# Performance work log

Measured on AMD Instinct MI355X. Metric: run time of the kernel, lower is better.

## Reference

```python
import jax, jax.numpy as jnp
import numpy as np

N_NODES = 50000
N_EDGES = 1600000
IN_FEATS = 128
HIDDEN = 128
N_CLASSES = 16
N_GRAPHS = 512


def setup_inputs() -> dict:
    key = jax.random.key(0)
    ks = jax.random.split(key, 10)
    features = jax.random.normal(ks[0], (N_NODES, IN_FEATS), dtype=jnp.float32)
    src = jax.random.randint(ks[1], (N_EDGES,), 0, N_NODES, dtype=jnp.int32)
    dst = jax.random.randint(ks[2], (N_EDGES,), 0, N_NODES, dtype=jnp.int32)
    graph_ids = jnp.sort(jax.random.randint(ks[3], (N_NODES,), 0, N_GRAPHS, dtype=jnp.int32))
    # GraphConv weights (glorot-ish scaling) and biases
    W1 = jax.random.normal(ks[4], (IN_FEATS, HIDDEN), dtype=jnp.float32) / np.sqrt(IN_FEATS)
    b1 = jnp.zeros((HIDDEN,), dtype=jnp.float32)
    W2 = jax.random.normal(ks[5], (HIDDEN, HIDDEN), dtype=jnp.float32) / np.sqrt(HIDDEN)
    b2 = jnp.zeros((HIDDEN,), dtype=jnp.float32)
    Wf = jax.random.normal(ks[6], (HIDDEN, N_CLASSES), dtype=jnp.float32) / np.sqrt(HIDDEN)
    bf = jnp.zeros((N_CLASSES,), dtype=jnp.float32)
    return {"features": features, "W1": W1, "b1": b1, "W2": W2, "b2": b2,
            "Wf": Wf, "bf": bf, "src": src, "dst": dst, "graph_ids": graph_ids}


def _graph_conv(h, W, b, src, dst, norm_out, norm_in):
    # DGL GraphConv, norm='both': h' = D_in^{-1/2} * A^T * (D_out^{-1/2} * h) @ W + b
    h = h * norm_out[:, None]              # [N, d] scale by src out-degree
    agg = jax.ops.segment_sum(h[src], dst, num_segments=N_NODES)  # gather-scatter SpMM
    agg = agg * norm_in[:, None]
    return agg @ W + b


def reference(features, W1, b1, W2, b2, Wf, bf, src, dst, graph_ids):
    ones_e = jnp.ones((N_EDGES,), dtype=features.dtype)
    deg_out = jax.ops.segment_sum(ones_e, src, num_segments=N_NODES)
    deg_in = jax.ops.segment_sum(ones_e, dst, num_segments=N_NODES)
    norm_out = jnp.where(deg_out > 0, jax.lax.rsqrt(jnp.maximum(deg_out, 1.0)), 0.0)
    norm_in = jnp.where(deg_in > 0, jax.lax.rsqrt(jnp.maximum(deg_in, 1.0)), 0.0)

    x = jax.nn.relu(_graph_conv(features, W1, b1, src, dst, norm_out, norm_in))
    x = jax.nn.relu(_graph_conv(x, W2, b2, src, dst, norm_out, norm_in))

    # mean_nodes: per-graph mean pooling over batched graph
    sums = jax.ops.segment_sum(x, graph_ids, num_segments=N_GRAPHS)   # [G, d]
    counts = jax.ops.segment_sum(jnp.ones((N_NODES,), dtype=x.dtype), graph_ids,
                                 num_segments=N_GRAPHS)
    pooled = sums / jnp.maximum(counts, 1.0)[:, None]
    return pooled @ Wf + bf
```

## Files before the change

### kernel.cpp

```cpp
#include <hip/hip_runtime.h>

#define N_NODES 50000
#define N_EDGES 1600000
#define FEATS 128
#define N_GRAPHS 512
#define N_CLASSES 16

#define NC 400
#define CE 4000
#define NB 391
#define SLAB 4608
#define CSLAB 5632
#define ZROW 50000

typedef __attribute__((ext_vector_type(8))) short bf16x8;
typedef __attribute__((ext_vector_type(4))) float f32x4;

__device__ inline unsigned bf16_rne_bits(float x) {
    unsigned u = __float_as_uint(x);
    return (u + 0x7FFFu + ((u >> 16) & 1u)) >> 16;
}
__device__ inline unsigned pack_bf16(float a, float b) {
    return (bf16_rne_bits(b) << 16) | bf16_rne_bits(a);
}
__device__ inline float bf16lo(unsigned u) { return __uint_as_float(u << 16); }
__device__ inline float bf16hi(unsigned u) { return __uint_as_float(u & 0xFFFF0000u); }

__global__ __launch_bounds__(256) void countrank_kernel(
        const int* __restrict__ src, const int* __restrict__ dst,
        unsigned* __restrict__ ranks, unsigned* __restrict__ cntD, unsigned* __restrict__ cntS,
        const float* __restrict__ W1, const float* __restrict__ W2,
        unsigned short* __restrict__ t1h, unsigned short* __restrict__ t1l,
        unsigned short* __restrict__ t2h, unsigned short* __restrict__ t2l) {
    __shared__ unsigned hD[NB], hS[NB];
    if (blockIdx.x >= NC) {
        int b = blockIdx.x - NC;
        const float* W = (b < 64) ? W1 : W2;
        unsigned short* th = (b < 64) ? t1h : t2h;
        unsigned short* tl = (b < 64) ? t1l : t2l;
        int idx = (b & 63) * 256 + threadIdx.x;
        int k = idx >> 7;
        int col = idx & 127;
        float w = W[idx];
        unsigned hb = bf16_rne_bits(w);
        float hf = __uint_as_float(hb << 16);
        unsigned lb = bf16_rne_bits(w - hf);
        th[col * 128 + k] = (unsigned short)hb;
        tl[col * 128 + k] = (unsigned short)lb;
        return;
    }
    for (int i = threadIdx.x; i < NB; i += 256) { hD[i] = 0; hS[i] = 0; }
    __syncthreads();
    int c = blockIdx.x;
    int lo = c * CE;
    for (int i = lo + threadIdx.x; i < lo + CE; i += 256) {
        int d = dst[i];
        int s = src[i];
        unsigned rD = atomicAdd(&hD[d >> 7], 1u);
        unsigned rS = atomicAdd(&hS[s >> 7], 1u);
        ranks[i] = rD | (rS << 16);
    }
    __syncthreads();
    for (int i = threadIdx.x; i < NB; i += 256) {
        cntD[c * NB + i] = hD[i];
        cntS[c * NB + i] = hS[i];
    }
}

__global__ __launch_bounds__(512) void colscan_kernel(
        unsigned* __restrict__ cntD, unsigned* __restrict__ cntS,
        unsigned* __restrict__ totD, unsigned* __restrict__ totS) {
    int bb = blockIdx.x;
    unsigned* cnt = (bb < NB) ? cntD : cntS;
    unsigned* tot = (bb < NB) ? totD : totS;
    int col = (bb < NB) ? bb : bb - NB;
    __shared__ unsigned buf[512];
    int t = threadIdx.x;
    unsigned v = (t < NC) ? cnt[t * NB + col] : 0;
    buf[t] = v;
    __syncthreads();
    for (int off = 1; off < 512; off <<= 1) {
        unsigned add = (t >= off) ? buf[t - off] : 0;
        __syncthreads();
        buf[t] += add;
        __syncthreads();
    }
    if (t < NC) cnt[t * NB + col] = buf[t] - v;
    if (t == NC - 1) tot[col] = buf[t];
}

__global__ __launch_bounds__(256) void scatter_kernel(
        const int* __restrict__ src, const int* __restrict__ dst,
        const unsigned* __restrict__ ranks,
        const unsigned* __restrict__ colbaseD, const unsigned* __restrict__ colbaseS,
        unsigned* __restrict__ arenaD, unsigned char* __restrict__ arenaS) {
    __shared__ unsigned cbD[NB], cbS[NB];
    int c = blockIdx.x;
    for (int i = threadIdx.x; i < NB; i += 256) {
        cbD[i] = colbaseD[c * NB + i];
        cbS[i] = colbaseS[c * NB + i];
    }
    __syncthreads();
    int lo = c * CE;
    for (int i = lo + threadIdx.x; i < lo + CE; i += 256) {
        int d = dst[i];
        int s = src[i];
        unsigned rr = ranks[i];
        unsigned posD = (unsigned)(d >> 7) * SLAB + cbD[d >> 7] + (rr & 0xFFFFu);
        arenaD[posD] = (unsigned)s | ((unsigned)(d & 127) << 16);
        unsigned posS = (unsigned)(s >> 7) * SLAB + cbS[s >> 7] + (rr >> 16);
        arenaS[posS] = (unsigned char)(s & 127);
    }
}

__global__ __launch_bounds__(256) void finalize_kernel(
        const unsigned* __restrict__ arenaD, const unsigned* __restrict__ totD,
        const unsigned char* __restrict__ arenaS, const unsigned* __restrict__ totS,
        unsigned short* __restrict__ csr, unsigned* __restrict__ row_start,
        unsigned* __restrict__ cnt_in, unsigned* __restrict__ deg_out) {
    int b = blockIdx.x;
    __shared__ unsigned h[128], h2[128], loc[128], sbuf[128];
    __shared__ unsigned short stag[CSLAB];
    int t = threadIdx.x;
    if (t < 128) { h[t] = 0; h2[t] = 0; }
    for (int i = t; i < CSLAB; i += 256) stag[i] = (unsigned short)ZROW;
    __syncthreads();
    unsigned nbS = totS[b];
    const unsigned char* slabS = arenaS + (size_t)b * SLAB;
    for (unsigned i = t; i < nbS; i += 256) atomicAdd(&h2[slabS[i]], 1u);
    __syncthreads();
    if (t < 128) {
        int ss = b * 128 + t;
        if (ss < N_NODES) deg_out[ss] = h2[t];
        h2[t] = 0;
    }
    __syncthreads();
    unsigned nb = totD[b];
    const unsigned* slab = arenaD + (size_t)b * SLAB;
    for (unsigned i = t; i < nb; i += 256) atomicAdd(&h[slab[i] >> 16], 1u);
    __syncthreads();
    unsigned myv = 0;
    if (t < 128) { myv = (h[t] + 7u) & ~7u; sbuf[t] = myv; }
    __syncthreads();
    for (int off = 1; off < 128; off <<= 1) {
        unsigned add = 0;
        if (t < 128 && t >= off) add = sbuf[t - off];
        __syncthreads();
        if (t < 128) sbuf[t] += add;
        __syncthreads();
    }
    if (t < 128) {
        loc[t] = sbuf[t] - myv;
        int dd = b * 128 + t;
        if (dd < N_NODES) {
            cnt_in[dd] = h[t];
            row_start[dd] = (unsigned)b * CSLAB + loc[t];
        }
    }
    __syncthreads();
    for (unsigned i = t; i < nb; i += 256) {
        unsigned e = slab[i];
        unsigned dl = e >> 16;
        unsigned r = atomicAdd(&h2[dl], 1u);
        stag[loc[dl] + r] = (unsigned short)(e & 0xFFFFu);
    }
    __syncthreads();
    unsigned tot_aligned = sbuf[127];
    unsigned short* g = csr + (size_t)b * CSLAB;
    for (unsigned i = t; i < tot_aligned; i += 256) g[i] = stag[i];
}

__global__ void norm_prescale_kernel(const unsigned* __restrict__ deg_out,
                                     const unsigned* __restrict__ cnt_in,
                                     const float* __restrict__ X, unsigned* __restrict__ Xs,
                                     float* __restrict__ norm_in_a, float* __restrict__ norm_out_a,
                                     const int* __restrict__ gids,
                                     int* __restrict__ gstart, int* __restrict__ gend) {
    int gid = blockIdx.x * blockDim.x + threadIdx.x;
    if (gid >= (N_NODES + 1) * 16) return;
    int node = gid >> 4;
    int c = gid & 15;
    if (node >= N_NODES) {
        uint4 z = {0u, 0u, 0u, 0u};
        *reinterpret_cast<uint4*>(Xs + (size_t)node * (FEATS / 2) + c * 4) = z;
        return;
    }
    unsigned d0 = deg_out[node];
    float no = d0 > 0 ? rsqrtf((float)d0) : 0.f;
    float4 a0 = *reinterpret_cast<const float4*>(X + (size_t)node * FEATS + c * 8);
    float4 a1 = *reinterpret_cast<const float4*>(X + (size_t)node * FEATS + c * 8 + 4);
    uint4 p;
    p.x = pack_bf16(a0.x * no, a0.y * no);
    p.y = pack_bf16(a0.z * no, a0.w * no);
    p.z = pack_bf16(a1.x * no, a1.y * no);
    p.w = pack_bf16(a1.z * no, a1.w * no);
    *reinterpret_cast<uint4*>(Xs + (size_t)node * (FEATS / 2) + c * 4) = p;
    if (c == 0) {
        norm_out_a[node] = no;
        unsigned d1 = cnt_in[node];
        norm_in_a[node] = d1 > 0 ? rsqrtf((float)d1) : 0.f;
        int g = gids[node];
        if (node == 0 || gids[node - 1] != g) gstart[g] = node;
        if (node == N_NODES - 1 || gids[node + 1] != g) gend[g] = node + 1;
    }
}

__global__ __launch_bounds__(256) void agg_kernel(const unsigned* __restrict__ Xs,
        const unsigned short* __restrict__ csr, const unsigned* __restrict__ row_start,
        const unsigned* __restrict__ cnt_in, unsigned* __restrict__ out) {
    int b = blockIdx.x;
    int h = b & 1;
    int node = (b >> 1) * 8 + (threadIdx.x >> 5);
    if (node >= N_NODES) return;
    int lane = threadIdx.x & 31;
    unsigned n = cnt_in[node];
    const unsigned short* row = csr + row_start[node];
    const unsigned base = h * 32 + lane;
    float alo = 0.f, ahi = 0.f;
    unsigned n8 = (n + 7u) & ~7u;
    for (unsigned j = 0; j < n8; j += 8) {
        uint4 iv = *reinterpret_cast<const uint4*>(row + j);
        unsigned s0 = iv.x & 0xFFFFu, s1 = iv.x >> 16;
        unsigned s2 = iv.y & 0xFFFFu, s3 = iv.y >> 16;
        unsigned s4 = iv.z & 0xFFFFu, s5 = iv.z >> 16;
        unsigned s6 = iv.w & 0xFFFFu, s7 = iv.w >> 16;
        unsigned g0 = Xs[(size_t)s0 * 64 + base];
        unsigned g1 = Xs[(size_t)s1 * 64 + base];
        unsigned g2 = Xs[(size_t)s2 * 64 + base];
        unsigned g3 = Xs[(size_t)s3 * 64 + base];
        unsigned g4 = Xs[(size_t)s4 * 64 + base];
        unsigned g5 = Xs[(size_t)s5 * 64 + base];
        unsigned g6 = Xs[(size_t)s6 * 64 + base];
        unsigned g7 = Xs[(size_t)s7 * 64 + base];
        alo += ((bf16lo(g0) + bf16lo(g1)) + (bf16lo(g2) + bf16lo(g3)))
             + ((bf16lo(g4) + bf16lo(g5)) + (bf16lo(g6) + bf16lo(g7)));
        ahi += ((bf16hi(g0) + bf16hi(g1)) + (bf16hi(g2) + bf16hi(g3)))
             + ((bf16hi(g4) + bf16hi(g5)) + (bf16hi(g6) + bf16hi(g7)));
    }
    out[(size_t)node * 64 + base] = pack_bf16(alo, ahi);
}

template <bool BF16_OUT>
__global__ __launch_bounds__(256) void gemm_kernel(
        const unsigned* __restrict__ A,
        const unsigned short* __restrict__ Wth, const unsigned short* __restrict__ Wtl,
        const float* __restrict__ bias, const float* __restrict__ norm_in,
        const float* __restrict__ post, float* __restrict__ out_f32,
        unsigned short* __restrict__ out_b16, int n_rows) {
    __shared__ unsigned sWh[128 * 68];
    __shared__ unsigned sWl[128 * 68];
    {
        const uint4* gh = reinterpret_cast<const uint4*>(Wth);
        const uint4* gl = reinterpret_cast<const uint4*>(Wtl);
        for (int i = threadIdx.x; i < 2048; i += 256) {
            int col = i >> 4, q = i & 15;
            *reinterpret_cast<uint4*>(sWh + col * 68 + q * 4) = gh[i];
            *reinterpret_cast<uint4*>(sWl + col * 68 + q * 4) = gl[i];
        }
    }
    __syncthreads();

    const int l = threadIdx.x & 63;
    const int w = threadIdx.x >> 6;
    const int rl = l & 15;
    const int kg = l >> 4;
    const int row0 = blockIdx.x * 64 + w * 16;

    int row_a = row0 + rl;
    if (row_a >= n_rows) row_a = n_rows - 1;
    const uint4* Arow = reinterpret_cast<const uint4*>(A + (size_t)row_a * 64);

    f32x4 acc[8];
#pragma unroll
    for (int ct = 0; ct < 8; ++ct) acc[ct] = (f32x4){0.f, 0.f, 0.f, 0.f};

#pragma unroll
    for (int s = 0; s < 4; ++s) {
        bf16x8 af = __builtin_bit_cast(bf16x8, Arow[4 * s + kg]);
#pragma unroll
        for (int ct = 0; ct < 8; ++ct) {
            int colb = ct * 16 + rl;
            bf16x8 bh = __builtin_bit_cast(bf16x8,
                *reinterpret_cast<const uint4*>(sWh + colb * 68 + 16 * s + 4 * kg));
            bf16x8 bl = __builtin_bit_cast(bf16x8,
                *reinterpret_cast<const uint4*>(sWl + colb * 68 + 16 * s + 4 * kg));
            acc[ct] = __builtin_amdgcn_mfma_f32_16x16x32_bf16(af, bl, acc[ct], 0, 0, 0);
            acc[ct] = __builtin_amdgcn_mfma_f32_16x16x32_bf16(af, bh, acc[ct], 0, 0, 0);
        }
    }

    const int rb = row0 + kg * 4;
    float ni[4], po[4];
#pragma unroll
    for (int j = 0; j < 4; ++j) {
        int r = rb + j;
        bool v = r < n_rows;
        ni[j] = v ? norm_in[r] : 0.f;
        po[j] = (BF16_OUT && v) ? post[r] : 1.f;
    }
#pragma unroll
    for (int ct = 0; ct < 8; ++ct) {
        int col = ct * 16 + rl;
        float bc = bias[col];
#pragma unroll
        for (int j = 0; j < 4; ++j) {
            int r = rb + j;
            if (r < n_rows) {
                float o = fmaxf(fmaf(acc[ct][j], ni[j], bc), 0.f);
                if (BF16_OUT)
                    out_b16[(size_t)r * 128 + col] = (unsigned short)bf16_rne_bits(o * po[j]);
                else
                    out_f32[(size_t)r * 128 + col] = o;
            }
        }
    }
}

__global__ __launch_bounds__(256) void pool_final_kernel(
        const float* __restrict__ H, const int* __restrict__ gstart,
        const int* __restrict__ gend, const float* __restrict__ Wf,
        const float* __restrict__ bf, float* __restrict__ out) {
    int g = blockIdx.x;
    int s = gstart[g];
    int e = gend[g];
    int f = threadIdx.x & 127;
    int h = threadIdx.x >> 7;
    float acc = 0.f;
    for (int r = s + h; r < e; r += 2) acc += H[(size_t)r * FEATS + f];
    __shared__ float tmp[256];
    __shared__ float pooled[FEATS];
    tmp[threadIdx.x] = acc;
    __syncthreads();
    if (threadIdx.x < FEATS) {
        float inv = 1.0f / fmaxf((float)(e - s), 1.0f);
        pooled[threadIdx.x] = (tmp[threadIdx.x] + tmp[threadIdx.x + 128]) * inv;
    }
    __syncthreads();
    if (threadIdx.x < N_CLASSES) {
        int c = threadIdx.x;
        float d = bf[c];
        for (int k = 0; k < FEATS; ++k) d = fmaf(pooled[k], Wf[k * N_CLASSES + c], d);
        out[g * N_CLASSES + c] = d;
    }
}

extern "C" void kernel_launch(void* const* d_in, const int* in_sizes, int n_in,
                              void* d_out, int out_size, void* d_ws, size_t ws_size,
                              hipStream_t stream) {
    const float* features = (const float*)d_in[0];
    const float* W1 = (const float*)d_in[1];
    const float* b1 = (const float*)d_in[2];
    const float* W2 = (const float*)d_in[3];
    const float* b2 = (const float*)d_in[4];
    const float* Wf = (const float*)d_in[5];
    const float* bf = (const float*)d_in[6];
    const int* src = (const int*)d_in[7];
    const int* dst = (const int*)d_in[8];
    const int* gids = (const int*)d_in[9];
    float* out = (float*)d_out;

    char* wp = (char*)d_ws;
    auto alloc = [&wp](size_t bytes) {
        char* p = wp;
        wp += (bytes + 255) & ~(size_t)255;
        return p;
    };
    unsigned* buf0u = (unsigned*)alloc(((size_t)N_NODES + 1) * 64 * 4);
    float* buf1 = (float*)alloc((size_t)N_NODES * FEATS * 4 + 256);
    unsigned* B16 = (unsigned*)buf1;
    unsigned short* B16s = (unsigned short*)buf1;
    float* norm_in_a = (float*)alloc(N_NODES * 4);
    float* norm_out_a = (float*)alloc(N_NODES * 4);
    unsigned* deg_out = (unsigned*)alloc(N_NODES * 4);
    unsigned* cnt_in = (unsigned*)alloc(N_NODES * 4);
    unsigned* row_start = (unsigned*)alloc(N_NODES * 4);
    int* gboth = (int*)alloc(2 * N_GRAPHS * 4);
    int* gstart = gboth;
    int* gend = gboth + N_GRAPHS;
    unsigned short* t1h = (unsigned short*)alloc(4 * 16384 * 2);
    unsigned short* t1l = t1h + 16384;
    unsigned short* t2h = t1l + 16384;
    unsigned short* t2l = t2h + 16384;
    unsigned* cntD = (unsigned*)alloc((size_t)NC * NB * 4);
    unsigned* cntS = (unsigned*)alloc((size_t)NC * NB * 4);
    unsigned* totD = (unsigned*)alloc(NB * 4);
    unsigned* totS = (unsigned*)alloc(NB * 4);
    unsigned* arenaD = (unsigned*)alloc((size_t)NB * SLAB * 4);
    unsigned* ranks = (unsigned*)alloc((size_t)N_EDGES * 4);
    unsigned short* csr = (unsigned short*)ranks;
    unsigned char* arenaS = (unsigned char*)alloc((size_t)NB * SLAB);

    (void)hipMemsetAsync(gboth, 0, 2 * N_GRAPHS * sizeof(int), stream);

    countrank_kernel<<<NC + 128, 256, 0, stream>>>(src, dst, ranks, cntD, cntS,
                                                   W1, W2, t1h, t1l, t2h, t2l);
    colscan_kernel<<<2 * NB, 512, 0, stream>>>(cntD, cntS, totD, totS);
    scatter_kernel<<<NC, 256, 0, stream>>>(src, dst, ranks, cntD, cntS, arenaD, arenaS);
    finalize_kernel<<<NB, 256, 0, stream>>>(arenaD, totD, arenaS, totS,
                                            csr, row_start, cnt_in, deg_out);

    norm_prescale_kernel<<<((N_NODES + 1) * 16 + 255) / 256, 256, 0, stream>>>(
        deg_out, cnt_in, features, B16, norm_in_a, norm_out_a, gids, gstart, gend);

    const int agg_blocks = 2 * ((N_NODES + 7) / 8);
    const int gemm_blocks = (N_NODES + 63) / 64;

    agg_kernel<<<agg_blocks, 256, 0, stream>>>(B16, csr, row_start, cnt_in, buf0u);
    gemm_kernel<true><<<gemm_blocks, 256, 0, stream>>>(
        buf0u, t1h, t1l, b1, norm_in_a, norm_out_a, nullptr, B16s, N_NODES);

    agg_kernel<<<agg_blocks, 256, 0, stream>>>(B16, csr, row_start, cnt_in, buf0u);
    gemm_kernel<false><<<gemm_blocks, 256, 0, stream>>>(
        buf0u, t2h, t2l, b2, norm_in_a, nullptr, buf1, nullptr, N_NODES);

    pool_final_kernel<<<N_GRAPHS, 256, 0, stream>>>(buf1, gstart, gend, Wf, bf, out);
}
```

Measured before the change: 219.5 us.

## Split CSR rows by source half and widen aggregation gathers to uint2

The CSR build now partitions each destination row into two padded segments, one for sources below a midpoint and one for sources above. Both in-degree counts are packed into a single word. The aggregation kernel now gives each node 16 lanes, and each lane loads two packed words (four bf16 values) per neighbour. This halves gather instruction count and may improve cache locality by grouping source ranges. The cost is extra padding entries, which means more zero-row gathers and a tighter fit in the fixed CSLAB staging area.

Result: slower. 226.0 us (+2.9%).

```diff
diff --git a/kernel.cpp b/kernel.cpp
--- a/kernel.cpp
+++ b/kernel.cpp
@@ -12,6 +12,7 @@
 #define SLAB 4608
 #define CSLAB 5632
 #define ZROW 50000
+#define SRC_MID 25000
 
 typedef __attribute__((ext_vector_type(8))) short bf16x8;
 typedef __attribute__((ext_vector_type(4))) float f32x4;
@@ -117,30 +118,37 @@
         const unsigned* __restrict__ arenaD, const unsigned* __restrict__ totD,
         const unsigned char* __restrict__ arenaS, const unsigned* __restrict__ totS,
         unsigned short* __restrict__ csr, unsigned* __restrict__ row_start,
-        unsigned* __restrict__ cnt_in, unsigned* __restrict__ deg_out) {
+        unsigned* __restrict__ cnt2, unsigned* __restrict__ deg_out) {
     int b = blockIdx.x;
-    __shared__ unsigned h[128], h2[128], loc[128], sbuf[128];
+    __shared__ unsigned hlo[128], hhi[128], clo[128], chi[128], loc[128], sbuf[128];
     __shared__ unsigned short stag[CSLAB];
     int t = threadIdx.x;
-    if (t < 128) { h[t] = 0; h2[t] = 0; }
+    if (t < 128) { hlo[t] = 0; hhi[t] = 0; clo[t] = 0; chi[t] = 0; }
     for (int i = t; i < CSLAB; i += 256) stag[i] = (unsigned short)ZROW;
     __syncthreads();
     unsigned nbS = totS[b];
     const unsigned char* slabS = arenaS + (size_t)b * SLAB;
-    for (unsigned i = t; i < nbS; i += 256) atomicAdd(&h2[slabS[i]], 1u);
+    for (unsigned i = t; i < nbS; i += 256) atomicAdd(&clo[slabS[i]], 1u);
     __syncthreads();
     if (t < 128) {
         int ss = b * 128 + t;
-        if (ss < N_NODES) deg_out[ss] = h2[t];
-        h2[t] = 0;
+        if (ss < N_NODES) deg_out[ss] = clo[t];
+        clo[t] = 0;
     }
     __syncthreads();
     unsigned nb = totD[b];
     const unsigned* slab = arenaD + (size_t)b * SLAB;
-    for (unsigned i = t; i < nb; i += 256) atomicAdd(&h[slab[i] >> 16], 1u);
+    for (unsigned i = t; i < nb; i += 256) {
+        unsigned e = slab[i];
+        if ((e & 0xFFFFu) < SRC_MID) atomicAdd(&hlo[e >> 16], 1u);
+        else atomicAdd(&hhi[e >> 16], 1u);
+    }
     __syncthreads();
     unsigned myv = 0;
-    if (t < 128) { myv = (h[t] + 7u) & ~7u; sbuf[t] = myv; }
+    if (t < 128) {
+        myv = ((hlo[t] + 7u) & ~7u) + ((hhi[t] + 7u) & ~7u);
+        sbuf[t] = myv;
+    }
     __syncthreads();
     for (int off = 1; off < 128; off <<= 1) {
         unsigned add = 0;
@@ -153,7 +161,7 @@
         loc[t] = sbuf[t] - myv;
         int dd = b * 128 + t;
         if (dd < N_NODES) {
-            cnt_in[dd] = h[t];
+            cnt2[dd] = hlo[t] | (hhi[t] << 16);
             row_start[dd] = (unsigned)b * CSLAB + loc[t];
         }
     }
@@ -161,8 +169,11 @@
     for (unsigned i = t; i < nb; i += 256) {
         unsigned e = slab[i];
         unsigned dl = e >> 16;
-        unsigned r = atomicAdd(&h2[dl], 1u);
-        stag[loc[dl] + r] = (unsigned short)(e & 0xFFFFu);
+        unsigned s = e & 0xFFFFu;
+        unsigned pos;
+        if (s < SRC_MID) pos = loc[dl] + atomicAdd(&clo[dl], 1u);
+        else pos = loc[dl] + ((hlo[dl] + 7u) & ~7u) + atomicAdd(&chi[dl], 1u);
+        stag[pos] = (unsigned short)s;
     }
     __syncthreads();
     unsigned tot_aligned = sbuf[127];
@@ -171,7 +182,7 @@
 }
 
 __global__ void norm_prescale_kernel(const unsigned* __restrict__ deg_out,
-                                     const unsigned* __restrict__ cnt_in,
+                                     const unsigned* __restrict__ cnt2,
                                      const float* __restrict__ X, unsigned* __restrict__ Xs,
                                      float* __restrict__ norm_in_a, float* __restrict__ norm_out_a,
                                      const int* __restrict__ gids,
@@ -197,7 +208,8 @@
     *reinterpret_cast<uint4*>(Xs + (size_t)node * (FEATS / 2) + c * 4) = p;
     if (c == 0) {
         norm_out_a[node] = no;
-        unsigned d1 = cnt_in[node];
+        unsigned c2 = cnt2[node];
+        unsigned d1 = (c2 & 0xFFFFu) + (c2 >> 16);
         norm_in_a[node] = d1 > 0 ? rsqrtf((float)d1) : 0.f;
         int g = gids[node];
         if (node == 0 || gids[node - 1] != g) gstart[g] = node;
@@ -207,37 +219,44 @@
 
 __global__ __launch_bounds__(256) void agg_kernel(const unsigned* __restrict__ Xs,
         const unsigned short* __restrict__ csr, const unsigned* __restrict__ row_start,
-        const unsigned* __restrict__ cnt_in, unsigned* __restrict__ out) {
+        const unsigned* __restrict__ cnt2, unsigned* __restrict__ out) {
     int b = blockIdx.x;
     int h = b & 1;
-    int node = (b >> 1) * 8 + (threadIdx.x >> 5);
+    int node = (b >> 1) * 16 + (threadIdx.x >> 4);
     if (node >= N_NODES) return;
-    int lane = threadIdx.x & 31;
-    unsigned n = cnt_in[node];
+    int lane = threadIdx.x & 15;
+    unsigned c2 = cnt2[node];
+    unsigned ntot = (((c2 & 0xFFFFu) + 7u) & ~7u) + (((c2 >> 16) + 7u) & ~7u);
     const unsigned short* row = csr + row_start[node];
-    const unsigned base = h * 32 + lane;
-    float alo = 0.f, ahi = 0.f;
-    unsigned n8 = (n + 7u) & ~7u;
-    for (unsigned j = 0; j < n8; j += 8) {
+    const unsigned base = h * 32 + lane * 2;
+    float a0 = 0.f, a1 = 0.f, a2 = 0.f, a3 = 0.f;
+    for (unsigned j = 0; j < ntot; j += 8) {
         uint4 iv = *reinterpret_cast<const uint4*>(row + j);
         unsigned s0 = iv.x & 0xFFFFu, s1 = iv.x >> 16;
         unsigned s2 = iv.y & 0xFFFFu, s3 = iv.y >> 16;
         unsigned s4 = iv.z & 0xFFFFu, s5 = iv.z >> 16;
         unsigned s6 = iv.w & 0xFFFFu, s7 = iv.w >> 16;
-        unsigned g0 = Xs[(size_t)s0 * 64 + base];
-        unsigned g1 = Xs[(size_t)s1 * 64 + base];
-        unsigned g2 = Xs[(size_t)s2 * 64 + base];
-        unsigned g3 = Xs[(size_t)s3 * 64 + base];
-        unsigned g4 = Xs[(size_t)s4 * 64 + base];
-        unsigned g5 = Xs[(size_t)s5 * 64 + base];
-        unsigned g6 = Xs[(size_t)s6 * 64 + base];
-        unsigned g7 = Xs[(size_t)s7 * 64 + base];
-        alo += ((bf16lo(g0) + bf16lo(g1)) + (bf16lo(g2) + bf16lo(g3)))
-             + ((bf16lo(g4) + bf16lo(g5)) + (bf16lo(g6) + bf16lo(g7)));
-        ahi += ((bf16hi(g0) + bf16hi(g1)) + (bf16hi(g2) + bf16hi(g3)))
-             + ((bf16hi(g4) + bf16hi(g5)) + (bf16hi(g6) + bf16hi(g7)));
-    }
-    out[(size_t)node * 64 + base] = pack_bf16(alo, ahi);
+        uint2 g0 = *reinterpret_cast<const uint2*>(Xs + (size_t)s0 * 64 + base);
+        uint2 g1 = *reinterpret_cast<const uint2*>(Xs + (size_t)s1 * 64 + base);
+        uint2 g2 = *reinterpret_cast<const uint2*>(Xs + (size_t)s2 * 64 + base);
+        uint2 g3 = *reinterpret_cast<const uint2*>(Xs + (size_t)s3 * 64 + base);
+        uint2 g4 = *reinterpret_cast<const uint2*>(Xs + (size_t)s4 * 64 + base);
+        uint2 g5 = *reinterpret_cast<const uint2*>(Xs + (size_t)s5 * 64 + base);
+        uint2 g6 = *reinterpret_cast<const uint2*>(Xs + (size_t)s6 * 64 + base);
+        uint2 g7 = *reinterpret_cast<const uint2*>(Xs + (size_t)s7 * 64 + base);
+        a0 += ((bf16lo(g0.x) + bf16lo(g1.x)) + (bf16lo(g2.x) + bf16lo(g3.x)))
+            + ((bf16lo(g4.x) + bf16lo(g5.x)) + (bf16lo(g6.x) + bf16lo(g7.x)));
+        a1 += ((bf16hi(g0.x) + bf16hi(g1.x)) + (bf16hi(g2.x) + bf16hi(g3.x)))
+            + ((bf16hi(g4.x) + bf16hi(g5.x)) + (bf16hi(g6.x) + bf16hi(g7.x)));
+        a2 += ((bf16lo(g0.y) + bf16lo(g1.y)) + (bf16lo(g2.y) + bf16lo(g3.y)))
+            + ((bf16lo(g4.y) + bf16lo(g5.y)) + (bf16lo(g6.y) + bf16lo(g7.y)));
+        a3 += ((bf16hi(g0.y) + bf16hi(g1.y)) + (bf16hi(g2.y) + bf16hi(g3.y)))
+            + ((bf16hi(g4.y) + bf16hi(g5.y)) + (bf16hi(g6.y) + bf16hi(g7.y)));
+    }
+    uint2 o;
+    o.x = pack_bf16(a0, a1);
+    o.y = pack_bf16(a2, a3);
+    *reinterpret_cast<uint2*>(out + (size_t)node * 64 + base) = o;
 }
 
 template <bool BF16_OUT>
@@ -372,7 +391,7 @@
     float* norm_in_a = (float*)alloc(N_NODES * 4);
     float* norm_out_a = (float*)alloc(N_NODES * 4);
     unsigned* deg_out = (unsigned*)alloc(N_NODES * 4);
-    unsigned* cnt_in = (unsigned*)alloc(N_NODES * 4);
+    unsigned* cnt2 = (unsigned*)alloc(N_NODES * 4);
     unsigned* row_start = (unsigned*)alloc(N_NODES * 4);
     int* gboth = (int*)alloc(2 * N_GRAPHS * 4);
     int* gstart = gboth;
@@ -397,19 +416,19 @@
     colscan_kernel<<<2 * NB, 512, 0, stream>>>(cntD, cntS, totD, totS);
     scatter_kernel<<<NC, 256, 0, stream>>>(src, dst, ranks, cntD, cntS, arenaD, arenaS);
     finalize_kernel<<<NB, 256, 0, stream>>>(arenaD, totD, arenaS, totS,
-                                            csr, row_start, cnt_in, deg_out);
+                                            csr, row_start, cnt2, deg_out);
 
     norm_prescale_kernel<<<((N_NODES + 1) * 16 + 255) / 256, 256, 0, stream>>>(
-        deg_out, cnt_in, features, B16, norm_in_a, norm_out_a, gids, gstart, gend);
-
-    const int agg_blocks = 2 * ((N_NODES + 7) / 8);
+        deg_out, cnt2, features, B16, norm_in_a, norm_out_a, gids, gstart, gend);
+
+    const int agg_blocks = 2 * ((N_NODES + 15) / 16);
     const int gemm_blocks = (N_NODES + 63) / 64;
 
-    agg_kernel<<<agg_blocks, 256, 0, stream>>>(B16, csr, row_start, cnt_in, buf0u);
+    agg_kernel<<<agg_blocks, 256, 0, stream>>>(B16, csr, row_start, cnt2, buf0u);
     gemm_kernel<true><<<gemm_blocks, 256, 0, stream>>>(
         buf0u, t1h, t1l, b1, norm_in_a, norm_out_a, nullptr, B16s, N_NODES);
 
-    agg_kernel<<<agg_blocks, 256, 0, stream>>>(B16, csr, row_start, cnt_in, buf0u);
+    agg_kernel<<<agg_blocks, 256, 0, stream>>>(B16, csr, row_start, cnt2, buf0u);
     gemm_kernel<false><<<gemm_blocks, 256, 0, stream>>>(
         buf0u, t2h, t2l, b2, norm_in_a, nullptr, buf1, nullptr, N_NODES);
 
```

## Fuse norm/prescale into finalize and split CSR rows by source half

Applied to the files above, without the earlier changes.

The norm_prescale kernel is merged into finalize_kernel, which now computes degrees, norms, graph bounds and the bf16 prescaled features per 128-node slab, removing one launch and the degree round trip through global memory. Each destination row's neighbor list is also split into two padded segments, sources below 25000 and sources at or above it, with both counts packed into one word. This groups gathers by source range to improve cache locality, at the cost of extra padding per row. The aggregation loop is unrolled by two.

Result: faster. 212.4 us (-3.2%).

```diff
diff --git a/kernel.cpp b/kernel.cpp
--- a/kernel.cpp
+++ b/kernel.cpp
@@ -12,6 +12,7 @@
 #define SLAB 4608
 #define CSLAB 5632
 #define ZROW 50000
+#define SRC_MID 25000
 
 typedef __attribute__((ext_vector_type(8))) short bf16x8;
 typedef __attribute__((ext_vector_type(4))) float f32x4;
@@ -117,30 +118,36 @@
         const unsigned* __restrict__ arenaD, const unsigned* __restrict__ totD,
         const unsigned char* __restrict__ arenaS, const unsigned* __restrict__ totS,
         unsigned short* __restrict__ csr, unsigned* __restrict__ row_start,
-        unsigned* __restrict__ cnt_in, unsigned* __restrict__ deg_out) {
+        unsigned* __restrict__ cnt2,
+        const float* __restrict__ X, unsigned* __restrict__ Xs,
+        float* __restrict__ norm_in_a, float* __restrict__ norm_out_a,
+        const int* __restrict__ gids, int* __restrict__ gstart, int* __restrict__ gend) {
     int b = blockIdx.x;
-    __shared__ unsigned h[128], h2[128], loc[128], sbuf[128];
+    __shared__ unsigned hlo[128], hhi[128], clo[128], chi[128], loc[128], sbuf[128], degs[128];
     __shared__ unsigned short stag[CSLAB];
     int t = threadIdx.x;
-    if (t < 128) { h[t] = 0; h2[t] = 0; }
+    if (t < 128) { hlo[t] = 0; hhi[t] = 0; clo[t] = 0; chi[t] = 0; }
     for (int i = t; i < CSLAB; i += 256) stag[i] = (unsigned short)ZROW;
     __syncthreads();
     unsigned nbS = totS[b];
     const unsigned char* slabS = arenaS + (size_t)b * SLAB;
-    for (unsigned i = t; i < nbS; i += 256) atomicAdd(&h2[slabS[i]], 1u);
-    __syncthreads();
-    if (t < 128) {
-        int ss = b * 128 + t;
-        if (ss < N_NODES) deg_out[ss] = h2[t];
-        h2[t] = 0;
-    }
+    for (unsigned i = t; i < nbS; i += 256) atomicAdd(&clo[slabS[i]], 1u);
+    __syncthreads();
+    if (t < 128) { degs[t] = clo[t]; clo[t] = 0; }
     __syncthreads();
     unsigned nb = totD[b];
     const unsigned* slab = arenaD + (size_t)b * SLAB;
-    for (unsigned i = t; i < nb; i += 256) atomicAdd(&h[slab[i] >> 16], 1u);
+    for (unsigned i = t; i < nb; i += 256) {
+        unsigned e = slab[i];
+        if ((e & 0xFFFFu) < SRC_MID) atomicAdd(&hlo[e >> 16], 1u);
+        else atomicAdd(&hhi[e >> 16], 1u);
+    }
     __syncthreads();
     unsigned myv = 0;
-    if (t < 128) { myv = (h[t] + 7u) & ~7u; sbuf[t] = myv; }
+    if (t < 128) {
+        myv = ((hlo[t] + 7u) & ~7u) + ((hhi[t] + 7u) & ~7u);
+        sbuf[t] = myv;
+    }
     __syncthreads();
     for (int off = 1; off < 128; off <<= 1) {
         unsigned add = 0;
@@ -153,7 +160,7 @@
         loc[t] = sbuf[t] - myv;
         int dd = b * 128 + t;
         if (dd < N_NODES) {
-            cnt_in[dd] = h[t];
+            cnt2[dd] = hlo[t] | (hhi[t] << 16);
             row_start[dd] = (unsigned)b * CSLAB + loc[t];
         }
     }
@@ -161,64 +168,65 @@
     for (unsigned i = t; i < nb; i += 256) {
         unsigned e = slab[i];
         unsigned dl = e >> 16;
-        unsigned r = atomicAdd(&h2[dl], 1u);
-        stag[loc[dl] + r] = (unsigned short)(e & 0xFFFFu);
+        unsigned s = e & 0xFFFFu;
+        unsigned pos;
+        if (s < SRC_MID) pos = loc[dl] + atomicAdd(&clo[dl], 1u);
+        else pos = loc[dl] + ((hlo[dl] + 7u) & ~7u) + atomicAdd(&chi[dl], 1u);
+        stag[pos] = (unsigned short)s;
     }
     __syncthreads();
     unsigned tot_aligned = sbuf[127];
     unsigned short* g = csr + (size_t)b * CSLAB;
     for (unsigned i = t; i < tot_aligned; i += 256) g[i] = stag[i];
-}
-
-__global__ void norm_prescale_kernel(const unsigned* __restrict__ deg_out,
-                                     const unsigned* __restrict__ cnt_in,
-                                     const float* __restrict__ X, unsigned* __restrict__ Xs,
-                                     float* __restrict__ norm_in_a, float* __restrict__ norm_out_a,
-                                     const int* __restrict__ gids,
-                                     int* __restrict__ gstart, int* __restrict__ gend) {
-    int gid = blockIdx.x * blockDim.x + threadIdx.x;
-    if (gid >= (N_NODES + 1) * 16) return;
-    int node = gid >> 4;
-    int c = gid & 15;
-    if (node >= N_NODES) {
-        uint4 z = {0u, 0u, 0u, 0u};
-        *reinterpret_cast<uint4*>(Xs + (size_t)node * (FEATS / 2) + c * 4) = z;
-        return;
-    }
-    unsigned d0 = deg_out[node];
-    float no = d0 > 0 ? rsqrtf((float)d0) : 0.f;
-    float4 a0 = *reinterpret_cast<const float4*>(X + (size_t)node * FEATS + c * 8);
-    float4 a1 = *reinterpret_cast<const float4*>(X + (size_t)node * FEATS + c * 8 + 4);
-    uint4 p;
-    p.x = pack_bf16(a0.x * no, a0.y * no);
-    p.y = pack_bf16(a0.z * no, a0.w * no);
-    p.z = pack_bf16(a1.x * no, a1.y * no);
-    p.w = pack_bf16(a1.z * no, a1.w * no);
-    *reinterpret_cast<uint4*>(Xs + (size_t)node * (FEATS / 2) + c * 4) = p;
-    if (c == 0) {
-        norm_out_a[node] = no;
-        unsigned d1 = cnt_in[node];
-        norm_in_a[node] = d1 > 0 ? rsqrtf((float)d1) : 0.f;
-        int g = gids[node];
-        if (node == 0 || gids[node - 1] != g) gstart[g] = node;
-        if (node == N_NODES - 1 || gids[node + 1] != g) gend[g] = node + 1;
+    for (int task = t; task < 128 * 16; task += 256) {
+        int nl = task >> 4;
+        int c = task & 15;
+        int node = b * 128 + nl;
+        if (node < N_NODES) {
+            unsigned d0 = degs[nl];
+            float no = d0 > 0 ? rsqrtf((float)d0) : 0.f;
+            float4 a0 = *reinterpret_cast<const float4*>(X + (size_t)node * FEATS + c * 8);
+            float4 a1 = *reinterpret_cast<const float4*>(X + (size_t)node * FEATS + c * 8 + 4);
+            uint4 p;
+            p.x = pack_bf16(a0.x * no, a0.y * no);
+            p.y = pack_bf16(a0.z * no, a0.w * no);
+            p.z = pack_bf16(a1.x * no, a1.y * no);
+            p.w = pack_bf16(a1.z * no, a1.w * no);
+            *reinterpret_cast<uint4*>(Xs + (size_t)node * (FEATS / 2) + c * 4) = p;
+        } else if (node == ZROW) {
+            uint4 z = {0u, 0u, 0u, 0u};
+            *reinterpret_cast<uint4*>(Xs + (size_t)node * (FEATS / 2) + c * 4) = z;
+        }
+    }
+    if (t < 128) {
+        int node = b * 128 + t;
+        if (node < N_NODES) {
+            unsigned d0 = degs[t];
+            norm_out_a[node] = d0 > 0 ? rsqrtf((float)d0) : 0.f;
+            unsigned d1 = hlo[t] + hhi[t];
+            norm_in_a[node] = d1 > 0 ? rsqrtf((float)d1) : 0.f;
+            int g2 = gids[node];
+            if (node == 0 || gids[node - 1] != g2) gstart[g2] = node;
+            if (node == N_NODES - 1 || gids[node + 1] != g2) gend[g2] = node + 1;
+        }
     }
 }
 
 __global__ __launch_bounds__(256) void agg_kernel(const unsigned* __restrict__ Xs,
         const unsigned short* __restrict__ csr, const unsigned* __restrict__ row_start,
-        const unsigned* __restrict__ cnt_in, unsigned* __restrict__ out) {
+        const unsigned* __restrict__ cnt2, unsigned* __restrict__ out) {
     int b = blockIdx.x;
     int h = b & 1;
     int node = (b >> 1) * 8 + (threadIdx.x >> 5);
     if (node >= N_NODES) return;
     int lane = threadIdx.x & 31;
-    unsigned n = cnt_in[node];
+    unsigned c2 = cnt2[node];
+    unsigned ntot = (((c2 & 0xFFFFu) + 7u) & ~7u) + (((c2 >> 16) + 7u) & ~7u);
     const unsigned short* row = csr + row_start[node];
     const unsigned base = h * 32 + lane;
     float alo = 0.f, ahi = 0.f;
-    unsigned n8 = (n + 7u) & ~7u;
-    for (unsigned j = 0; j < n8; j += 8) {
+#pragma unroll 2
+    for (unsigned j = 0; j < ntot; j += 8) {
         uint4 iv = *reinterpret_cast<const uint4*>(row + j);
         unsigned s0 = iv.x & 0xFFFFu, s1 = iv.x >> 16;
         unsigned s2 = iv.y & 0xFFFFu, s3 = iv.y >> 16;
@@ -371,8 +379,7 @@
     unsigned short* B16s = (unsigned short*)buf1;
     float* norm_in_a = (float*)alloc(N_NODES * 4);
     float* norm_out_a = (float*)alloc(N_NODES * 4);
-    unsigned* deg_out = (unsigned*)alloc(N_NODES * 4);
-    unsigned* cnt_in = (unsigned*)alloc(N_NODES * 4);
+    unsigned* cnt2 = (unsigned*)alloc(N_NODES * 4);
     unsigned* row_start = (unsigned*)alloc(N_NODES * 4);
     int* gboth = (int*)alloc(2 * N_GRAPHS * 4);
     int* gstart = gboth;
@@ -397,19 +404,18 @@
     colscan_kernel<<<2 * NB, 512, 0, stream>>>(cntD, cntS, totD, totS);
     scatter_kernel<<<NC, 256, 0, stream>>>(src, dst, ranks, cntD, cntS, arenaD, arenaS);
     finalize_kernel<<<NB, 256, 0, stream>>>(arenaD, totD, arenaS, totS,
-                                            csr, row_start, cnt_in, deg_out);
-
-    norm_prescale_kernel<<<((N_NODES + 1) * 16 + 255) / 256, 256, 0, stream>>>(
-        deg_out, cnt_in, features, B16, norm_in_a, norm_out_a, gids, gstart, gend);
+                                            csr, row_start, cnt2,
+                                            features, B16, norm_in_a, norm_out_a,
+                                            gids, gstart, gend);
 
     const int agg_blocks = 2 * ((N_NODES + 7) / 8);
     const int gemm_blocks = (N_NODES + 63) / 64;
 
-    agg_kernel<<<agg_blocks, 256, 0, stream>>>(B16, csr, row_start, cnt_in, buf0u);
+    agg_kernel<<<agg_blocks, 256, 0, stream>>>(B16, csr, row_start, cnt2, buf0u);
     gemm_kernel<true><<<gemm_blocks, 256, 0, stream>>>(
         buf0u, t1h, t1l, b1, norm_in_a, norm_out_a, nullptr, B16s, N_NODES);
 
-    agg_kernel<<<agg_blocks, 256, 0, stream>>>(B16, csr, row_start, cnt_in, buf0u);
+    agg_kernel<<<agg_blocks, 256, 0, stream>>>(B16, csr, row_start, cnt2, buf0u);
     gemm_kernel<false><<<gemm_blocks, 256, 0, stream>>>(
         buf0u, t2h, t2l, b2, norm_in_a, nullptr, buf1, nullptr, N_NODES);
 
```
